# Kernel tuning notes

Hardware: AMD Instinct MI355X
Metric: run time of the kernel (lower is better)

## Reference

```python
import jax, jax.numpy as jnp
import numpy as np


def setup_inputs() -> dict:
    key = jax.random.key(0)
    k1, k2 = jax.random.split(key)
    z_e_x = jax.random.normal(k1, (4096, 16, 128), dtype=jnp.float32)
    codebook = jax.random.normal(k2, (1024, 128), dtype=jnp.float32)
    return {"z_e_x": z_e_x, "codebook": codebook}


def reference(z_e_x, codebook):
    # VQStraightThrough.forward: nearest-codebook quantization in fp32.
    B, N, C = z_e_x.shape
    x = z_e_x.astype(jnp.float32).reshape(B * N, C)          # [BN, C]
    cb = codebook.astype(jnp.float32)                        # [K, C]
    inputs_sq = jnp.sum(x * x, axis=1, keepdims=True)        # [BN, 1]
    codebook_sq = jnp.sum(cb * cb, axis=1)                   # [K]
    l2_dis = inputs_sq + codebook_sq - 2.0 * (x @ cb.T)      # [BN, K]
    flat_idx = jnp.argmin(l2_dis, axis=1)                    # [BN] int
    min_vals = jnp.min(l2_dis, axis=1)                       # [BN]
    idx = flat_idx.reshape(B, N)
    distances = min_vals.reshape(B, N).astype(z_e_x.dtype)
    codes = cb[flat_idx].reshape(B, N, C).astype(z_e_x.dtype)  # gather
    return codes, flat_idx, idx, distances
```

## Files before the change

### kernel.cpp

```cpp
#include <hip/hip_runtime.h>
#include <math.h>
#include <stdint.h>

#define C        128
#define KCODES   1024
#define TPB      256
#define ROWS_PB  128
#define NCHUNK   64
#define NCHUNKS  (KCODES / NCHUNK)
#define BSTRIDE  272
#define EPS_TRIG 0.25f

typedef __attribute__((ext_vector_type(8))) short bf16x8_t;
typedef __attribute__((ext_vector_type(4))) float f32x4_t;

static __device__ __forceinline__ uint32_t bf16_rne(float f) {
    uint32_t u = __float_as_uint(f);
    return (u + 0x7FFFu + ((u >> 16) & 1u)) >> 16;
}
static __device__ __forceinline__ float bf16_hi_f(float f) {
    return __uint_as_float(bf16_rne(f) << 16);
}

__global__ void cb_split_kernel(const float* __restrict__ cb,
                                uint16_t* __restrict__ cbh,
                                uint16_t* __restrict__ cbl) {
    int i = blockIdx.x * blockDim.x + threadIdx.x;
    if (i >= KCODES * C) return;
    float f = cb[i];
    uint32_t h = bf16_rne(f);
    float lo = f - __uint_as_float(h << 16);
    cbh[i] = (uint16_t)h;
    cbl[i] = (uint16_t)bf16_rne(lo);
}

__global__ void cbsq_kernel(const float* __restrict__ cb, float* __restrict__ cbsq) {
    const int k = blockIdx.x * blockDim.x + threadIdx.x;
    if (k >= KCODES) return;
    const float4* cp = (const float4*)(cb + (size_t)k * C);
    float sx = 0.f, sy = 0.f, sz = 0.f, sw = 0.f;
    #pragma unroll
    for (int i = 0; i < C / 4; ++i) {
        float4 v = cp[i];
        sx += v.x * v.x; sy += v.y * v.y;
        sz += v.z * v.z; sw += v.w * v.w;
    }
    cbsq[k] = (sx + sy) + (sz + sw);
}

#define SLOTS(OP) OP(0,0) OP(0,1) OP(0,2) OP(0,3) OP(1,0) OP(1,1) OP(1,2) OP(1,3)
#define MFMA_BF16 __builtin_amdgcn_mfma_f32_16x16x32_bf16

__global__ __launch_bounds__(TPB, 3)
void vq_mfma_kernel(const float* __restrict__ x,
                    const float* __restrict__ cb,
                    const uint16_t* __restrict__ cbh,
                    const uint16_t* __restrict__ cbl,
                    const float* __restrict__ cq,
                    float* __restrict__ out_codes,
                    float* __restrict__ out_fidx,
                    float* __restrict__ out_idx,
                    float* __restrict__ out_dist,
                    int rows)
{
    __shared__ __align__(16) uint8_t s_buf[NCHUNK * 2 * BSTRIDE];
    __shared__ float s_cq[NCHUNK];
    __shared__ float s_v1[ROWS_PB], s_v2[ROWS_PB];
    __shared__ int   s_k1[ROWS_PB], s_k2[ROWS_PB];

    const int t    = threadIdx.x;
    const int lane = t & 63;
    const int w    = t >> 6;
    const int ln   = lane & 15;
    const int quad = lane >> 4;
    const int rowblock = blockIdx.x * ROWS_PB;

    #pragma unroll 4
    for (int i = 0; i < 16; ++i) {
        int fid = t + i * TPB;
        int row = fid >> 5;
        int kq  = fid & 31;
        int grow = rowblock + row;
        grow = grow < rows ? grow : rows - 1;
        float4 v = ((const float4*)x)[(size_t)grow * 32 + kq];
        uint32_t p0 = bf16_rne(v.x) | (bf16_rne(v.y) << 16);
        uint32_t p1 = bf16_rne(v.z) | (bf16_rne(v.w) << 16);
        *(uint2*)(s_buf + row * BSTRIDE + kq * 8) = make_uint2(p0, p1);
    }
    __syncthreads();

    const int arow0 = (w * 32 + ln) * BSTRIDE;
    const int arow1 = (w * 32 + 16 + ln) * BSTRIDE;
    bf16x8_t ah00, ah01, ah02, ah03, ah10, ah11, ah12, ah13;
    ah00 = *(const bf16x8_t*)(s_buf + arow0 + 0 * 64 + quad * 16);
    ah01 = *(const bf16x8_t*)(s_buf + arow0 + 1 * 64 + quad * 16);
    ah02 = *(const bf16x8_t*)(s_buf + arow0 + 2 * 64 + quad * 16);
    ah03 = *(const bf16x8_t*)(s_buf + arow0 + 3 * 64 + quad * 16);
    ah10 = *(const bf16x8_t*)(s_buf + arow1 + 0 * 64 + quad * 16);
    ah11 = *(const bf16x8_t*)(s_buf + arow1 + 1 * 64 + quad * 16);
    ah12 = *(const bf16x8_t*)(s_buf + arow1 + 2 * 64 + quad * 16);
    ah13 = *(const bf16x8_t*)(s_buf + arow1 + 3 * 64 + quad * 16);
    __syncthreads();

    #pragma unroll 4
    for (int i = 0; i < 16; ++i) {
        int fid = t + i * TPB;
        int row = fid >> 5;
        int kq  = fid & 31;
        int grow = rowblock + row;
        grow = grow < rows ? grow : rows - 1;
        float4 v = ((const float4*)x)[(size_t)grow * 32 + kq];
        uint32_t p0 = bf16_rne(v.x - bf16_hi_f(v.x)) | (bf16_rne(v.y - bf16_hi_f(v.y)) << 16);
        uint32_t p1 = bf16_rne(v.z - bf16_hi_f(v.z)) | (bf16_rne(v.w - bf16_hi_f(v.w)) << 16);
        *(uint2*)(s_buf + row * BSTRIDE + kq * 8) = make_uint2(p0, p1);
    }
    __syncthreads();

    bf16x8_t al00, al01, al02, al03, al10, al11, al12, al13;
    al00 = *(const bf16x8_t*)(s_buf + arow0 + 0 * 64 + quad * 16);
    al01 = *(const bf16x8_t*)(s_buf + arow0 + 1 * 64 + quad * 16);
    al02 = *(const bf16x8_t*)(s_buf + arow0 + 2 * 64 + quad * 16);
    al03 = *(const bf16x8_t*)(s_buf + arow0 + 3 * 64 + quad * 16);
    al10 = *(const bf16x8_t*)(s_buf + arow1 + 0 * 64 + quad * 16);
    al11 = *(const bf16x8_t*)(s_buf + arow1 + 1 * 64 + quad * 16);
    al12 = *(const bf16x8_t*)(s_buf + arow1 + 2 * 64 + quad * 16);
    al13 = *(const bf16x8_t*)(s_buf + arow1 + 3 * 64 + quad * 16);
    __syncthreads();

#define DECL(g,r) float v1_##g##r = INFINITY, v2_##g##r = INFINITY; int k1_##g##r = 0, k2_##g##r = 0;
    SLOTS(DECL)
#undef DECL

    #pragma unroll 1
    for (int chn = 0; chn < NCHUNKS; ++chn) {
        const int kbase = chn * NCHUNK;
        #pragma unroll
        for (int i = 0; i < 4; ++i) {
            int uid  = t + i * TPB;
            int code = uid >> 4, g = uid & 15;
            uint4 dh = ((const uint4*)cbh)[(size_t)(kbase + code) * 16 + g];
            *(uint4*)(s_buf + code * BSTRIDE + g * 16) = dh;
            uint4 dl = ((const uint4*)cbl)[(size_t)(kbase + code) * 16 + g];
            *(uint4*)(s_buf + NCHUNK * BSTRIDE + code * BSTRIDE + g * 16) = dl;
        }
        if (t < NCHUNK) s_cq[t] = cq[kbase + t];
        __syncthreads();

        const uint8_t* bbase  = s_buf + (size_t)ln * BSTRIDE + quad * 16;
        #pragma unroll
        for (int ct = 0; ct < 4; ++ct) {
            const uint8_t* bh_p = bbase + (size_t)ct * 16 * BSTRIDE;
            const uint8_t* bl_p = bh_p + NCHUNK * BSTRIDE;
            f32x4_t acc0 = {0.f, 0.f, 0.f, 0.f};
            f32x4_t acc1 = {0.f, 0.f, 0.f, 0.f};
#define KSTEP(kk) { \
            bf16x8_t bh = *(const bf16x8_t*)(bh_p + kk * 64); \
            bf16x8_t bl = *(const bf16x8_t*)(bl_p + kk * 64); \
            acc0 = MFMA_BF16(ah0##kk, bh, acc0, 0, 0, 0); \
            acc0 = MFMA_BF16(al0##kk, bh, acc0, 0, 0, 0); \
            acc0 = MFMA_BF16(ah0##kk, bl, acc0, 0, 0, 0); \
            acc1 = MFMA_BF16(ah1##kk, bh, acc1, 0, 0, 0); \
            acc1 = MFMA_BF16(al1##kk, bh, acc1, 0, 0, 0); \
            acc1 = MFMA_BF16(ah1##kk, bl, acc1, 0, 0, 0); }
            KSTEP(0) KSTEP(1) KSTEP(2) KSTEP(3)
#undef KSTEP
            const float cqv = s_cq[ct * 16 + ln];
            const int   kc  = kbase + ct * 16 + ln;
#define UPD(g,r) { \
            float s_ = fmaf(-2.0f, (g ? acc1 : acc0)[r], cqv); \
            bool c1_ = s_ < v1_##g##r; \
            bool c2_ = s_ < v2_##g##r; \
            v2_##g##r = c1_ ? v1_##g##r : (c2_ ? s_ : v2_##g##r); \
            k2_##g##r = c1_ ? k1_##g##r : (c2_ ? kc : k2_##g##r); \
            v1_##g##r = c1_ ? s_ : v1_##g##r; \
            k1_##g##r = c1_ ? kc : k1_##g##r; }
            SLOTS(UPD)
#undef UPD
        }
        __syncthreads();
    }

    for (int m_ = 1; m_ <= 8; m_ <<= 1) {
#define MRG(g,r) { \
        float ov1 = __shfl_xor(v1_##g##r, m_, 16); int ok1 = __shfl_xor(k1_##g##r, m_, 16); \
        float ov2 = __shfl_xor(v2_##g##r, m_, 16); int ok2 = __shfl_xor(k2_##g##r, m_, 16); \
        if (ov1 < v1_##g##r || (ov1 == v1_##g##r && ok1 < k1_##g##r)) { \
            if (v1_##g##r < ov2 || (v1_##g##r == ov2 && k1_##g##r < ok2)) { v2_##g##r = v1_##g##r; k2_##g##r = k1_##g##r; } \
            else { v2_##g##r = ov2; k2_##g##r = ok2; } \
            v1_##g##r = ov1; k1_##g##r = ok1; \
        } else if (ov1 < v2_##g##r || (ov1 == v2_##g##r && ok1 < k2_##g##r)) { \
            v2_##g##r = ov1; k2_##g##r = ok1; \
        } }
        SLOTS(MRG)
#undef MRG
    }
    if (ln == 0) {
#define WRT(g,r) { int rloc = w * 32 + g * 16 + quad * 4 + r; \
        s_v1[rloc] = v1_##g##r; s_v2[rloc] = v2_##g##r; \
        s_k1[rloc] = k1_##g##r; s_k2[rloc] = k2_##g##r; }
        SLOTS(WRT)
#undef WRT
    }
    __syncthreads();

    if (t < ROWS_PB) {
        int rowg = rowblock + t;
        const bool valid = rowg < rows;
        rowg = valid ? rowg : rows - 1;
        float v1 = s_v1[t], v2 = s_v2[t];
        int k1 = s_k1[t], k2 = s_k2[t];
        const float* xr = x + (size_t)rowg * C;

        float sx = 0.f, sy = 0.f, sz = 0.f, sw = 0.f;
        {
            const float4* xp = (const float4*)xr;
            #pragma unroll
            for (int i = 0; i < C / 4; ++i) {
                float4 v = xp[i];
                sx += v.x * v.x; sy += v.y * v.y;
                sz += v.z * v.z; sw += v.w * v.w;
            }
        }
        const float rs = (sx + sy) + (sz + sw);

        bool switched = false;
        double qwin = 0.0;
        if (v2 - v1 < EPS_TRIG) {
            const float* c1p = cb + (size_t)k1 * C;
            const float* c2p = cb + (size_t)k2 * C;
            double dot1 = 0.0, cq1 = 0.0, dot2 = 0.0, cq2 = 0.0;
            #pragma unroll 8
            for (int c = 0; c < C; ++c) {
                const double xc  = (double)xr[c];
                const double cv1 = (double)c1p[c];
                const double cv2 = (double)c2p[c];
                dot1 += xc * cv1;  cq1 += cv1 * cv1;
                dot2 += xc * cv2;  cq2 += cv2 * cv2;
            }
            const double q1 = cq1 - 2.0 * dot1;
            const double q2 = cq2 - 2.0 * dot2;
            if (q2 < q1 || (q2 == q1 && k2 < k1)) { k1 = k2; switched = true; qwin = q2; }
        }

        const float* c1p = cb + (size_t)k1 * C;
        float a = 0.f;
        #pragma unroll 16
        for (int c = 0; c < C; ++c) a = fmaf(xr[c], c1p[c], a);
        float d = (rs + cq[k1]) - 2.f * a;
        if (switched) d = (float)((double)rs + qwin);

        if (valid) {
            out_fidx[rowg] = (float)k1;
            out_idx[rowg]  = (float)k1;
            out_dist[rowg] = d;
        }
        s_k1[t] = k1;
    }
    __syncthreads();

    {
        const int r    = t >> 1;
        const int half = t & 1;
        const int rowg = rowblock + r;
        if (rowg < rows) {
            const int k1 = s_k1[r];
            const float4* src = (const float4*)(cb + (size_t)k1 * C) + half * 16;
            float4*       dst = (float4*)(out_codes + (size_t)rowg * C) + half * 16;
            #pragma unroll
            for (int i = 0; i < 16; ++i) dst[i] = src[i];
        }
    }
}

__global__ __launch_bounds__(TPB, 1)
void vq_nearest_fallback(const float* __restrict__ x,
                         const float* __restrict__ cb,
                         float* __restrict__ out_codes,
                         float* __restrict__ out_fidx,
                         float* __restrict__ out_idx,
                         float* __restrict__ out_dist,
                         int rows)
{
    __shared__ float s_cbsq[KCODES];
    const int t = threadIdx.x;
    for (int k = t; k < KCODES; k += TPB) {
        const float4* cp = (const float4*)(cb + (size_t)k * C);
        float sx = 0.f, sy = 0.f, sz = 0.f, sw = 0.f;
        #pragma unroll
        for (int i = 0; i < C / 4; ++i) {
            float4 v = cp[i];
            sx += v.x * v.x; sy += v.y * v.y; sz += v.z * v.z; sw += v.w * v.w;
        }
        s_cbsq[k] = (sx + sy) + (sz + sw);
    }
    __syncthreads();
    const int row = blockIdx.x * TPB + t;
    if (row >= rows) return;
    float xr[C];
    {
        const float4* xp = (const float4*)(x + (size_t)row * C);
        #pragma unroll
        for (int i = 0; i < C / 4; ++i) {
            float4 v = xp[i];
            xr[4*i+0] = v.x; xr[4*i+1] = v.y; xr[4*i+2] = v.z; xr[4*i+3] = v.w;
        }
    }
    float rs;
    {
        float sx = 0.f, sy = 0.f, sz = 0.f, sw = 0.f;
        #pragma unroll
        for (int i = 0; i < C / 4; ++i) {
            sx += xr[4*i+0]*xr[4*i+0]; sy += xr[4*i+1]*xr[4*i+1];
            sz += xr[4*i+2]*xr[4*i+2]; sw += xr[4*i+3]*xr[4*i+3];
        }
        rs = (sx + sy) + (sz + sw);
    }
    float v1 = INFINITY, v2 = INFINITY; int k1 = 0, k2 = 0;
    #pragma unroll 1
    for (int k0 = 0; k0 < KCODES; k0 += 4) {
        const float* c0 = cb + (size_t)k0 * C;
        float a0 = 0.f, a1 = 0.f, a2 = 0.f, a3 = 0.f;
        #pragma unroll
        for (int c = 0; c < C; ++c) {
            const float xc = xr[c];
            a0 = fmaf(xc, c0[c], a0);
            a1 = fmaf(xc, c0[C + c], a1);
            a2 = fmaf(xc, c0[2*C + c], a2);
            a3 = fmaf(xc, c0[3*C + c], a3);
        }
        const float d0 = (rs + s_cbsq[k0+0]) - 2.f * a0;
        const float d1 = (rs + s_cbsq[k0+1]) - 2.f * a1;
        const float d2 = (rs + s_cbsq[k0+2]) - 2.f * a2;
        const float d3 = (rs + s_cbsq[k0+3]) - 2.f * a3;
        #define UPDF(dv, ki)                                                 \
            if ((dv) < v1)      { v2 = v1; k2 = k1; v1 = (dv); k1 = (ki); } \
            else if ((dv) < v2) { v2 = (dv); k2 = (ki); }
        UPDF(d0, k0+0); UPDF(d1, k0+1); UPDF(d2, k0+2); UPDF(d3, k0+3);
        #undef UPDF
    }
    if (v2 - v1 < 0.125f) {
        const float* c1p = cb + (size_t)k1 * C;
        const float* c2p = cb + (size_t)k2 * C;
        double dot1 = 0.0, cq1 = 0.0, dot2 = 0.0, cq2 = 0.0;
        #pragma unroll 8
        for (int c = 0; c < C; ++c) {
            const double xc = (double)xr[c];
            const double cv1 = (double)c1p[c];
            const double cv2 = (double)c2p[c];
            dot1 += xc * cv1; cq1 += cv1 * cv1;
            dot2 += xc * cv2; cq2 += cv2 * cv2;
        }
        const double q1 = cq1 - 2.0 * dot1;
        const double q2 = cq2 - 2.0 * dot2;
        if (q2 < q1 || (q2 == q1 && k2 < k1)) { k1 = k2; v1 = (float)((double)rs + q2); }
    }
    {
        const float4* src = (const float4*)(cb + (size_t)k1 * C);
        float4* dst = (float4*)(out_codes + (size_t)row * C);
        #pragma unroll
        for (int i = 0; i < C / 4; ++i) dst[i] = src[i];
        out_fidx[row] = (float)k1;
        out_idx[row]  = (float)k1;
        out_dist[row] = v1;
    }
}

extern "C" void kernel_launch(void* const* d_in, const int* in_sizes, int n_in,
                              void* d_out, int out_size, void* d_ws, size_t ws_size,
                              hipStream_t stream) {
    const float* x  = (const float*)d_in[0];
    const float* cb = (const float*)d_in[1];
    const int rows = in_sizes[0] / C;

    float* out       = (float*)d_out;
    float* out_codes = out;
    float* out_fidx  = out + (size_t)rows * C;
    float* out_idx   = out_fidx + rows;
    float* out_dist  = out_idx + rows;

    const size_t cbh_off = 0;
    const size_t cbl_off = (size_t)KCODES * C * sizeof(uint16_t);
    const size_t cq_off  = cbl_off * 2;
    const size_t need    = cq_off + KCODES * sizeof(float);

    if (ws_size >= need) {
        uint16_t* cbh = (uint16_t*)((char*)d_ws + cbh_off);
        uint16_t* cbl = (uint16_t*)((char*)d_ws + cbl_off);
        float*    cq  = (float*)((char*)d_ws + cq_off);

        cb_split_kernel<<<(KCODES * C + TPB - 1) / TPB, TPB, 0, stream>>>(cb, cbh, cbl);
        cbsq_kernel<<<(KCODES + TPB - 1) / TPB, TPB, 0, stream>>>(cb, cq);

        const int grid = (rows + ROWS_PB - 1) / ROWS_PB;
        vq_mfma_kernel<<<grid, TPB, 0, stream>>>(x, cb, cbh, cbl, cq,
                                                 out_codes, out_fidx, out_idx,
                                                 out_dist, rows);
    } else {
        const int rowblocks = (rows + TPB - 1) / TPB;
        vq_nearest_fallback<<<rowblocks, TPB, 0, stream>>>(x, cb, out_codes, out_fidx,
                                                           out_idx, out_dist, rows);
    }
}
```

Baseline: 174.7 us.

## Fuse codebook prep kernels, single-pass x split, and break MFMA accumulator chains

Merges the codebook split and squared-norm kernels into one launch. Converts x to bf16 hi and lo halves in a single global read, storing both in an enlarged shared buffer. Uses four independent accumulators per row group instead of one serial chain of twelve MFMAs, summing them at the end, to expose instruction-level parallelism. Precomputes shared-memory offsets and global pointers for the codebook chunk loads. Lowers the launch-bounds occupancy hint from 3 to 2, since the larger shared buffer and extra accumulators raise per-block resource use.

```diff
diff --git a/kernel.cpp b/kernel.cpp
--- a/kernel.cpp
+++ b/kernel.cpp
@@ -9,6 +9,8 @@
 #define NCHUNK   64
 #define NCHUNKS  (KCODES / NCHUNK)
 #define BSTRIDE  272
+#define BHALF    (NCHUNK * BSTRIDE)
+#define ALO_OFF  (ROWS_PB * BSTRIDE)
 #define EPS_TRIG 0.25f
 
 typedef __attribute__((ext_vector_type(8))) short bf16x8_t;
@@ -22,36 +24,35 @@
     return __uint_as_float(bf16_rne(f) << 16);
 }
 
-__global__ void cb_split_kernel(const float* __restrict__ cb,
-                                uint16_t* __restrict__ cbh,
-                                uint16_t* __restrict__ cbl) {
-    int i = blockIdx.x * blockDim.x + threadIdx.x;
-    if (i >= KCODES * C) return;
-    float f = cb[i];
-    uint32_t h = bf16_rne(f);
-    float lo = f - __uint_as_float(h << 16);
-    cbh[i] = (uint16_t)h;
-    cbl[i] = (uint16_t)bf16_rne(lo);
-}
-
-__global__ void cbsq_kernel(const float* __restrict__ cb, float* __restrict__ cbsq) {
-    const int k = blockIdx.x * blockDim.x + threadIdx.x;
-    if (k >= KCODES) return;
-    const float4* cp = (const float4*)(cb + (size_t)k * C);
-    float sx = 0.f, sy = 0.f, sz = 0.f, sw = 0.f;
-    #pragma unroll
-    for (int i = 0; i < C / 4; ++i) {
-        float4 v = cp[i];
-        sx += v.x * v.x; sy += v.y * v.y;
-        sz += v.z * v.z; sw += v.w * v.w;
-    }
-    cbsq[k] = (sx + sy) + (sz + sw);
+__global__ void cb_prep_kernel(const float* __restrict__ cb,
+                               uint16_t* __restrict__ cbh,
+                               uint16_t* __restrict__ cbl,
+                               float* __restrict__ cbsq) {
+    const int i = blockIdx.x * blockDim.x + threadIdx.x;
+    if (i < KCODES * C) {
+        float f = cb[i];
+        uint32_t h = bf16_rne(f);
+        float lo = f - __uint_as_float(h << 16);
+        cbh[i] = (uint16_t)h;
+        cbl[i] = (uint16_t)bf16_rne(lo);
+    }
+    if (i < KCODES) {
+        const float4* cp = (const float4*)(cb + (size_t)i * C);
+        float sx = 0.f, sy = 0.f, sz = 0.f, sw = 0.f;
+        #pragma unroll
+        for (int j = 0; j < C / 4; ++j) {
+            float4 v = cp[j];
+            sx += v.x * v.x; sy += v.y * v.y;
+            sz += v.z * v.z; sw += v.w * v.w;
+        }
+        cbsq[i] = (sx + sy) + (sz + sw);
+    }
 }
 
 #define SLOTS(OP) OP(0,0) OP(0,1) OP(0,2) OP(0,3) OP(1,0) OP(1,1) OP(1,2) OP(1,3)
 #define MFMA_BF16 __builtin_amdgcn_mfma_f32_16x16x32_bf16
 
-__global__ __launch_bounds__(TPB, 3)
+__global__ __launch_bounds__(TPB, 2)
 void vq_mfma_kernel(const float* __restrict__ x,
                     const float* __restrict__ cb,
                     const uint16_t* __restrict__ cbh,
@@ -63,7 +64,7 @@
                     float* __restrict__ out_dist,
                     int rows)
 {
-    __shared__ __align__(16) uint8_t s_buf[NCHUNK * 2 * BSTRIDE];
+    __shared__ __align__(16) uint8_t s_buf[2 * ALO_OFF];
     __shared__ float s_cq[NCHUNK];
     __shared__ float s_v1[ROWS_PB], s_v2[ROWS_PB];
     __shared__ int   s_k1[ROWS_PB], s_k2[ROWS_PB];
@@ -85,13 +86,17 @@
         float4 v = ((const float4*)x)[(size_t)grow * 32 + kq];
         uint32_t p0 = bf16_rne(v.x) | (bf16_rne(v.y) << 16);
         uint32_t p1 = bf16_rne(v.z) | (bf16_rne(v.w) << 16);
-        *(uint2*)(s_buf + row * BSTRIDE + kq * 8) = make_uint2(p0, p1);
+        uint32_t q0 = bf16_rne(v.x - bf16_hi_f(v.x)) | (bf16_rne(v.y - bf16_hi_f(v.y)) << 16);
+        uint32_t q1 = bf16_rne(v.z - bf16_hi_f(v.z)) | (bf16_rne(v.w - bf16_hi_f(v.w)) << 16);
+        *(uint2*)(s_buf + row * BSTRIDE + kq * 8)           = make_uint2(p0, p1);
+        *(uint2*)(s_buf + ALO_OFF + row * BSTRIDE + kq * 8) = make_uint2(q0, q1);
     }
     __syncthreads();
 
     const int arow0 = (w * 32 + ln) * BSTRIDE;
     const int arow1 = (w * 32 + 16 + ln) * BSTRIDE;
     bf16x8_t ah00, ah01, ah02, ah03, ah10, ah11, ah12, ah13;
+    bf16x8_t al00, al01, al02, al03, al10, al11, al12, al13;
     ah00 = *(const bf16x8_t*)(s_buf + arow0 + 0 * 64 + quad * 16);
     ah01 = *(const bf16x8_t*)(s_buf + arow0 + 1 * 64 + quad * 16);
     ah02 = *(const bf16x8_t*)(s_buf + arow0 + 2 * 64 + quad * 16);
@@ -100,74 +105,68 @@
     ah11 = *(const bf16x8_t*)(s_buf + arow1 + 1 * 64 + quad * 16);
     ah12 = *(const bf16x8_t*)(s_buf + arow1 + 2 * 64 + quad * 16);
     ah13 = *(const bf16x8_t*)(s_buf + arow1 + 3 * 64 + quad * 16);
-    __syncthreads();
-
-    #pragma unroll 4
-    for (int i = 0; i < 16; ++i) {
-        int fid = t + i * TPB;
-        int row = fid >> 5;
-        int kq  = fid & 31;
-        int grow = rowblock + row;
-        grow = grow < rows ? grow : rows - 1;
-        float4 v = ((const float4*)x)[(size_t)grow * 32 + kq];
-        uint32_t p0 = bf16_rne(v.x - bf16_hi_f(v.x)) | (bf16_rne(v.y - bf16_hi_f(v.y)) << 16);
-        uint32_t p1 = bf16_rne(v.z - bf16_hi_f(v.z)) | (bf16_rne(v.w - bf16_hi_f(v.w)) << 16);
-        *(uint2*)(s_buf + row * BSTRIDE + kq * 8) = make_uint2(p0, p1);
-    }
-    __syncthreads();
-
-    bf16x8_t al00, al01, al02, al03, al10, al11, al12, al13;
-    al00 = *(const bf16x8_t*)(s_buf + arow0 + 0 * 64 + quad * 16);
-    al01 = *(const bf16x8_t*)(s_buf + arow0 + 1 * 64 + quad * 16);
-    al02 = *(const bf16x8_t*)(s_buf + arow0 + 2 * 64 + quad * 16);
-    al03 = *(const bf16x8_t*)(s_buf + arow0 + 3 * 64 + quad * 16);
-    al10 = *(const bf16x8_t*)(s_buf + arow1 + 0 * 64 + quad * 16);
-    al11 = *(const bf16x8_t*)(s_buf + arow1 + 1 * 64 + quad * 16);
-    al12 = *(const bf16x8_t*)(s_buf + arow1 + 2 * 64 + quad * 16);
-    al13 = *(const bf16x8_t*)(s_buf + arow1 + 3 * 64 + quad * 16);
+    al00 = *(const bf16x8_t*)(s_buf + ALO_OFF + arow0 + 0 * 64 + quad * 16);
+    al01 = *(const bf16x8_t*)(s_buf + ALO_OFF + arow0 + 1 * 64 + quad * 16);
+    al02 = *(const bf16x8_t*)(s_buf + ALO_OFF + arow0 + 2 * 64 + quad * 16);
+    al03 = *(const bf16x8_t*)(s_buf + ALO_OFF + arow0 + 3 * 64 + quad * 16);
+    al10 = *(const bf16x8_t*)(s_buf + ALO_OFF + arow1 + 0 * 64 + quad * 16);
+    al11 = *(const bf16x8_t*)(s_buf + ALO_OFF + arow1 + 1 * 64 + quad * 16);
+    al12 = *(const bf16x8_t*)(s_buf + ALO_OFF + arow1 + 2 * 64 + quad * 16);
+    al13 = *(const bf16x8_t*)(s_buf + ALO_OFF + arow1 + 3 * 64 + quad * 16);
     __syncthreads();
 
 #define DECL(g,r) float v1_##g##r = INFINITY, v2_##g##r = INFINITY; int k1_##g##r = 0, k2_##g##r = 0;
     SLOTS(DECL)
 #undef DECL
 
+    int lds_off[4];
+    #pragma unroll
+    for (int i = 0; i < 4; ++i) {
+        int uid = t + i * TPB;
+        lds_off[i] = (uid >> 4) * BSTRIDE + (uid & 15) * 16;
+    }
+    const uint4* gh = (const uint4*)cbh + t;
+    const uint4* gl = (const uint4*)cbl + t;
+
     #pragma unroll 1
     for (int chn = 0; chn < NCHUNKS; ++chn) {
         const int kbase = chn * NCHUNK;
         #pragma unroll
         for (int i = 0; i < 4; ++i) {
-            int uid  = t + i * TPB;
-            int code = uid >> 4, g = uid & 15;
-            uint4 dh = ((const uint4*)cbh)[(size_t)(kbase + code) * 16 + g];
-            *(uint4*)(s_buf + code * BSTRIDE + g * 16) = dh;
-            uint4 dl = ((const uint4*)cbl)[(size_t)(kbase + code) * 16 + g];
-            *(uint4*)(s_buf + NCHUNK * BSTRIDE + code * BSTRIDE + g * 16) = dl;
-        }
+            uint4 dh = gh[i * TPB];
+            uint4 dl = gl[i * TPB];
+            *(uint4*)(s_buf + lds_off[i])          = dh;
+            *(uint4*)(s_buf + BHALF + lds_off[i])  = dl;
+        }
+        gh += NCHUNK * 16;
+        gl += NCHUNK * 16;
         if (t < NCHUNK) s_cq[t] = cq[kbase + t];
         __syncthreads();
 
-        const uint8_t* bbase  = s_buf + (size_t)ln * BSTRIDE + quad * 16;
+        const uint8_t* bbase = s_buf + (size_t)ln * BSTRIDE + quad * 16;
         #pragma unroll
         for (int ct = 0; ct < 4; ++ct) {
             const uint8_t* bh_p = bbase + (size_t)ct * 16 * BSTRIDE;
-            const uint8_t* bl_p = bh_p + NCHUNK * BSTRIDE;
-            f32x4_t acc0 = {0.f, 0.f, 0.f, 0.f};
-            f32x4_t acc1 = {0.f, 0.f, 0.f, 0.f};
+            const uint8_t* bl_p = bh_p + BHALF;
+            f32x4_t a00 = {0,0,0,0}, a01 = {0,0,0,0}, a02 = {0,0,0,0}, a03 = {0,0,0,0};
+            f32x4_t a10 = {0,0,0,0}, a11 = {0,0,0,0}, a12 = {0,0,0,0}, a13 = {0,0,0,0};
 #define KSTEP(kk) { \
             bf16x8_t bh = *(const bf16x8_t*)(bh_p + kk * 64); \
             bf16x8_t bl = *(const bf16x8_t*)(bl_p + kk * 64); \
-            acc0 = MFMA_BF16(ah0##kk, bh, acc0, 0, 0, 0); \
-            acc0 = MFMA_BF16(al0##kk, bh, acc0, 0, 0, 0); \
-            acc0 = MFMA_BF16(ah0##kk, bl, acc0, 0, 0, 0); \
-            acc1 = MFMA_BF16(ah1##kk, bh, acc1, 0, 0, 0); \
-            acc1 = MFMA_BF16(al1##kk, bh, acc1, 0, 0, 0); \
-            acc1 = MFMA_BF16(ah1##kk, bl, acc1, 0, 0, 0); }
+            a0##kk = MFMA_BF16(ah0##kk, bh, a0##kk, 0, 0, 0); \
+            a0##kk = MFMA_BF16(al0##kk, bh, a0##kk, 0, 0, 0); \
+            a0##kk = MFMA_BF16(ah0##kk, bl, a0##kk, 0, 0, 0); \
+            a1##kk = MFMA_BF16(ah1##kk, bh, a1##kk, 0, 0, 0); \
+            a1##kk = MFMA_BF16(al1##kk, bh, a1##kk, 0, 0, 0); \
+            a1##kk = MFMA_BF16(ah1##kk, bl, a1##kk, 0, 0, 0); }
             KSTEP(0) KSTEP(1) KSTEP(2) KSTEP(3)
 #undef KSTEP
+            const f32x4_t sum0 = (a00 + a01) + (a02 + a03);
+            const f32x4_t sum1 = (a10 + a11) + (a12 + a13);
             const float cqv = s_cq[ct * 16 + ln];
             const int   kc  = kbase + ct * 16 + ln;
 #define UPD(g,r) { \
-            float s_ = fmaf(-2.0f, (g ? acc1 : acc0)[r], cqv); \
+            float s_ = fmaf(-2.0f, (g ? sum1[r] : sum0[r]), cqv); \
             bool c1_ = s_ < v1_##g##r; \
             bool c2_ = s_ < v2_##g##r; \
             v2_##g##r = c1_ ? v1_##g##r : (c2_ ? s_ : v2_##g##r); \
@@ -388,8 +387,7 @@
         uint16_t* cbl = (uint16_t*)((char*)d_ws + cbl_off);
         float*    cq  = (float*)((char*)d_ws + cq_off);
 
-        cb_split_kernel<<<(KCODES * C + TPB - 1) / TPB, TPB, 0, stream>>>(cb, cbh, cbl);
-        cbsq_kernel<<<(KCODES + TPB - 1) / TPB, TPB, 0, stream>>>(cb, cq);
+        cb_prep_kernel<<<(KCODES * C + TPB - 1) / TPB, TPB, 0, stream>>>(cb, cbh, cbl, cq);
 
         const int grid = (rows + ROWS_PB - 1) / ROWS_PB;
         vq_mfma_kernel<<<grid, TPB, 0, stream>>>(x, cb, cbh, cbl, cq,
```

Result: faster. 170.5 us (-2.4%).
